# Kernel optimization log

Hardware: AMD Instinct MI355X
Metric: run time of the kernel (lower is better)

The kernel has to match this reference:

```python
import jax, jax.numpy as jnp
import numpy as np

NUM_EXPERT = 32
IN_FEAT = 256
OUT_FEAT = 256
TOTAL_TOKENS = 524288
CAPACITY = 16896  # static per-expert pad, > max expected count


def setup_inputs() -> dict:
    key = jax.random.key(0)
    k_inp, k_w = jax.random.split(key)
    inp = jax.random.normal(k_inp, (TOTAL_TOKENS, IN_FEAT), dtype=jnp.float32)
    # weight initialized like nn.Linear (kaiming-uniform-ish); scale of randn is fine for a numeric baseline
    weight = jax.random.normal(k_w, (NUM_EXPERT, OUT_FEAT, IN_FEAT), dtype=jnp.float32) * (1.0 / np.sqrt(IN_FEAT))
    # variable-sized expert groups summing exactly to TOTAL_TOKENS (tokens assumed pre-sorted by expert)
    rng = np.random.default_rng(0)
    counts = rng.multinomial(TOTAL_TOKENS, np.ones(NUM_EXPERT) / NUM_EXPERT)
    assert counts.max() <= CAPACITY and counts.sum() == TOTAL_TOKENS
    fwd_expert_count = jnp.asarray(counts, dtype=jnp.int64)
    return {"inp": inp, "weight": weight, "fwd_expert_count": fwd_expert_count, "capacity": CAPACITY}


def reference(inp, weight, fwd_expert_count, capacity):
    # Grouped GEMM: for expert e, out[seg_e] = inp[seg_e] @ weight[e].T
    E = weight.shape[0]
    T = inp.shape[0]
    counts = fwd_expert_count.astype(jnp.int32)
    cum = jnp.cumsum(counts)                       # [E] inclusive prefix sums
    starts = cum - counts                          # [E] segment starts
    tok = jnp.arange(T, dtype=jnp.int32)
    eid = jnp.searchsorted(cum, tok, side='right') # [T] expert id per token
    pos = tok - starts[eid]                        # [T] slot within expert group
    # Scatter tokens into padded per-expert buffer [E, capacity, in]
    buf = jnp.zeros((E, capacity, inp.shape[1]), dtype=inp.dtype).at[eid, pos].set(inp)
    # Batched matmul against per-expert weights [E, out, in] -> [E, capacity, out]
    y = jnp.einsum('eci,eoi->eco', buf, weight)
    # Gather back to token order [T, out]
    return y[eid, pos]
```

## Files before the change

kernel.cpp:

```cpp
#include <hip/hip_runtime.h>
#include <cstdint>
#include <cstddef>

#define NEXPERT 32
#define KIN 256
#define NOUT 256
#define NTOK 524288
#define BM 64

typedef float f32x4 __attribute__((ext_vector_type(4)));
typedef __bf16 bf16x8 __attribute__((ext_vector_type(8)));
typedef unsigned short u16;
typedef u16 u16x8 __attribute__((ext_vector_type(8)));

union BF8 { u16x8 u; bf16x8 b; };

__device__ __forceinline__ u16 f2bf(float f) {
  unsigned u = __float_as_uint(f);
  return (u16)((u + 0x7FFFu + ((u >> 16) & 1u)) >> 16);
}

__global__ void conv_w_kernel(const float* __restrict__ w, u16* __restrict__ wb) {
  const int i = (blockIdx.x * 256 + threadIdx.x) * 4;
  const float4 v = *reinterpret_cast<const float4*>(w + i);
  ushort4 o;
  o.x = f2bf(v.x); o.y = f2bf(v.y); o.z = f2bf(v.z); o.w = f2bf(v.w);
  *reinterpret_cast<ushort4*>(wb + i) = o;
}

__device__ __forceinline__ void gload(const float4* ap4, int ks, float4 (&v)[4]) {
#pragma unroll
  for (int i = 0; i < 4; ++i) v[i] = ap4[ks * 16 + i];
}

__device__ __forceinline__ void cvtw(const float4 (&v)[4], char* rbase, int cb, int rx) {
  u16x8 h0, h1;
  h0[0]=f2bf(v[0].x); h0[1]=f2bf(v[0].y); h0[2]=f2bf(v[0].z); h0[3]=f2bf(v[0].w);
  h0[4]=f2bf(v[1].x); h0[5]=f2bf(v[1].y); h0[6]=f2bf(v[1].z); h0[7]=f2bf(v[1].w);
  h1[0]=f2bf(v[2].x); h1[1]=f2bf(v[2].y); h1[2]=f2bf(v[2].z); h1[3]=f2bf(v[2].w);
  h1[4]=f2bf(v[3].x); h1[5]=f2bf(v[3].y); h1[6]=f2bf(v[3].z); h1[7]=f2bf(v[3].w);
  *reinterpret_cast<u16x8*>(rbase + ((cb     ) ^ rx)) = h0;
  *reinterpret_cast<u16x8*>(rbase + ((cb + 16) ^ rx)) = h1;
}

template<bool WSBF>
__device__ __forceinline__ void ldb(const u16* wB, const float* wF, int ks, BF8 (&dst)[4][2]) {
  if (WSBF) {
#pragma unroll
    for (int n = 0; n < 4; ++n)
#pragma unroll
      for (int kk = 0; kk < 2; ++kk)
        dst[n][kk].u = *reinterpret_cast<const u16x8*>(wB + n * (16 * KIN) + ks * 64 + kk * 32);
  } else {
#pragma unroll
    for (int n = 0; n < 4; ++n)
#pragma unroll
      for (int kk = 0; kk < 2; ++kk) {
        const float4* p = reinterpret_cast<const float4*>(wF + n * (16 * KIN) + ks * 64 + kk * 32);
        const float4 x = p[0], y = p[1];
        u16x8 h;
        h[0]=f2bf(x.x); h[1]=f2bf(x.y); h[2]=f2bf(x.z); h[3]=f2bf(x.w);
        h[4]=f2bf(y.x); h[5]=f2bf(y.y); h[6]=f2bf(y.z); h[7]=f2bf(y.w);
        dst[n][kk].u = h;
      }
  }
}

__device__ __forceinline__ void compute(const char* abase, int lg, int arx,
                                        const BF8 (&bfr)[4][2], f32x4 (&acc)[4][4]) {
#pragma unroll
  for (int kk = 0; kk < 2; ++kk) {
    BF8 af[4];
#pragma unroll
    for (int m = 0; m < 4; ++m)
      af[m].u = *reinterpret_cast<const u16x8*>(
          abase + m * 2048 + ((kk * 64 + (lg << 4)) ^ arx));
#pragma unroll
    for (int m = 0; m < 4; ++m)
#pragma unroll
      for (int n = 0; n < 4; ++n)
        acc[m][n] = __builtin_amdgcn_mfma_f32_16x16x32_bf16(
            af[m].b, bfr[n][kk].b, acc[m][n], 0, 0, 0);
  }
}

template<bool WSBF>
__global__ __launch_bounds__(256)
void moe_gemm_kernel(const float* __restrict__ inp,
                     const float* __restrict__ w32,
                     const u16* __restrict__ wbf,
                     const int* __restrict__ counts,
                     float* __restrict__ out)
{
  __shared__ u16 sA0[BM * 64];
  __shared__ u16 sA1[BM * 64];
  __shared__ int sCum[NEXPERT + 1];

  const int tid  = threadIdx.x;
  const int lane = tid & 63;
  const int wv   = tid >> 6;
  const int l15  = lane & 15;
  const int lg   = lane >> 4;

  if (tid < 32) {
    const long long* c64 = reinterpret_cast<const long long*>(counts);
    const long long p0 = c64[0];
    const bool is64 = (p0 >= 0 && p0 < (1ll << 31));
    int c = is64 ? (int)c64[tid] : counts[tid];
#pragma unroll
    for (int d = 1; d < 32; d <<= 1) {
      int o = __shfl_up(c, d, 64);
      if (tid >= d) c += o;
    }
    sCum[tid + 1] = c;
    if (tid == 0) sCum[0] = 0;
  }
  __syncthreads();

  const int t0 = blockIdx.x * BM;
  const int t1 = t0 + BM;

  int ee;
  {
    const int v = (lane < NEXPERT) ? sCum[lane + 1] : 0x7fffffff;
    const unsigned long long m = __ballot(v <= t0);
    ee = __popcll(m);
  }

  const int srow = tid >> 2;
  const int scol = (tid & 3) << 4;
  const float4* ap4 =
      reinterpret_cast<const float4*>(inp + (size_t)(t0 + srow) * KIN + scol);
  char* const r0 = reinterpret_cast<char*>(sA0) + srow * 128;
  char* const r1 = reinterpret_cast<char*>(sA1) + srow * 128;
  const int rx = (srow & 7) << 4;
  const int cb = scol << 1;
  const int arx = (l15 & 7) << 4;
  const char* const a0 = reinterpret_cast<const char*>(sA0) + l15 * 128;
  const char* const a1 = reinterpret_cast<const char*>(sA1) + l15 * 128;

  int rb = t0;
  int e = ee;
  while (rb < t1) {
    const int re = min(t1, sCum[e + 1]);
    if (re > rb) {
      const size_t wro = ((size_t)e << 16) + (size_t)((wv << 6) + l15) * KIN + lg * 8;
      const u16*   wB  = wbf + wro;
      const float* wF  = w32 + wro;

      f32x4 acc[4][4];
      const f32x4 zero = {0.f, 0.f, 0.f, 0.f};
#pragma unroll
      for (int m = 0; m < 4; ++m)
#pragma unroll
        for (int n = 0; n < 4; ++n) acc[m][n] = zero;

      float4 va[4], vb[4];
      BF8 bA[4][2], bB[4][2];

      gload(ap4, 0, va);
      gload(ap4, 1, vb);
      ldb<WSBF>(wB, wF, 0, bA);
      __syncthreads();
      cvtw(va, r0, cb, rx);
      __syncthreads();

      ldb<WSBF>(wB, wF, 1, bB); cvtw(vb, r1, cb, rx); gload(ap4, 2, va);
      compute(a0, lg, arx, bA, acc);
      __syncthreads();
      ldb<WSBF>(wB, wF, 2, bA); cvtw(va, r0, cb, rx); gload(ap4, 3, vb);
      compute(a1, lg, arx, bB, acc);
      __syncthreads();
      ldb<WSBF>(wB, wF, 3, bB); cvtw(vb, r1, cb, rx);
      compute(a0, lg, arx, bA, acc);
      __syncthreads();
      compute(a1, lg, arx, bB, acc);

      const bool full = (rb == t0) & (re == t1);
      if (full) {
#pragma unroll
        for (int m = 0; m < 4; ++m) {
          const int rbase = t0 + (m << 4) + (lg << 2);
#pragma unroll
          for (int n = 0; n < 4; ++n) {
            float* op = out + (size_t)rbase * NOUT + (wv << 6) + (n << 4) + l15;
#pragma unroll
            for (int j = 0; j < 4; ++j) op[(size_t)j * NOUT] = acc[m][n][j];
          }
        }
      } else {
#pragma unroll
        for (int m = 0; m < 4; ++m) {
          const int rbase = t0 + (m << 4) + (lg << 2);
#pragma unroll
          for (int n = 0; n < 4; ++n) {
            float* op = out + (size_t)rbase * NOUT + (wv << 6) + (n << 4) + l15;
#pragma unroll
            for (int j = 0; j < 4; ++j) {
              const int rg = rbase + j;
              if (rg >= rb && rg < re) op[(size_t)j * NOUT] = acc[m][n][j];
            }
          }
        }
      }
    }
    rb = re > rb ? re : rb;
    ++e;
  }
}

extern "C" void kernel_launch(void* const* d_in, const int* in_sizes, int n_in,
                              void* d_out, int out_size, void* d_ws, size_t ws_size,
                              hipStream_t stream) {
  const float* inp    = (const float*)d_in[0];
  const float* w      = (const float*)d_in[1];
  const int*   counts = (const int*)d_in[2];
  float*       out    = (float*)d_out;

  const size_t wbytes = (size_t)NEXPERT * NOUT * KIN * 2;
  const bool usews = (ws_size >= wbytes);

  if (usews) {
    u16* wbf = (u16*)d_ws;
    const int total = NEXPERT * NOUT * KIN;
    conv_w_kernel<<<total / (256 * 4), 256, 0, stream>>>(w, wbf);
    moe_gemm_kernel<true><<<NTOK / BM, 256, 0, stream>>>(inp, w, wbf, counts, out);
  } else {
    moe_gemm_kernel<false><<<NTOK / BM, 256, 0, stream>>>(inp, w, nullptr, counts, out);
  }
}
```

Measured before the change: 272.7 us.

## Load A fragments directly from global into registers, removing LDS staging and barriers

```diff
diff --git a/kernel.cpp b/kernel.cpp
--- a/kernel.cpp
+++ b/kernel.cpp
@@ -28,59 +28,32 @@
   *reinterpret_cast<ushort4*>(wb + i) = o;
 }
 
-__device__ __forceinline__ void gload(const float4* ap4, int ks, float4 (&v)[4]) {
-#pragma unroll
-  for (int i = 0; i < 4; ++i) v[i] = ap4[ks * 16 + i];
+__device__ __forceinline__ void cvt8(const float4& x, const float4& y, BF8& o) {
+  o.u[0]=f2bf(x.x); o.u[1]=f2bf(x.y); o.u[2]=f2bf(x.z); o.u[3]=f2bf(x.w);
+  o.u[4]=f2bf(y.x); o.u[5]=f2bf(y.y); o.u[6]=f2bf(y.z); o.u[7]=f2bf(y.w);
 }
 
-__device__ __forceinline__ void cvtw(const float4 (&v)[4], char* rbase, int cb, int rx) {
-  u16x8 h0, h1;
-  h0[0]=f2bf(v[0].x); h0[1]=f2bf(v[0].y); h0[2]=f2bf(v[0].z); h0[3]=f2bf(v[0].w);
-  h0[4]=f2bf(v[1].x); h0[5]=f2bf(v[1].y); h0[6]=f2bf(v[1].z); h0[7]=f2bf(v[1].w);
-  h1[0]=f2bf(v[2].x); h1[1]=f2bf(v[2].y); h1[2]=f2bf(v[2].z); h1[3]=f2bf(v[2].w);
-  h1[4]=f2bf(v[3].x); h1[5]=f2bf(v[3].y); h1[6]=f2bf(v[3].z); h1[7]=f2bf(v[3].w);
-  *reinterpret_cast<u16x8*>(rbase + ((cb     ) ^ rx)) = h0;
-  *reinterpret_cast<u16x8*>(rbase + ((cb + 16) ^ rx)) = h1;
+__device__ __forceinline__ void loadA(const float* aBase, int cch, float4 (&r)[8]) {
+#pragma unroll
+  for (int m = 0; m < 4; ++m) {
+    const float* p = aBase + (size_t)(m * 16) * KIN + cch * 32;
+    r[2*m]   = *reinterpret_cast<const float4*>(p);
+    r[2*m+1] = *reinterpret_cast<const float4*>(p + 4);
+  }
 }
 
 template<bool WSBF>
-__device__ __forceinline__ void ldb(const u16* wB, const float* wF, int ks, BF8 (&dst)[4][2]) {
+__device__ __forceinline__ void loadB(const u16* wB, const float* wF, int cch, BF8 (&d)[4]) {
   if (WSBF) {
 #pragma unroll
     for (int n = 0; n < 4; ++n)
-#pragma unroll
-      for (int kk = 0; kk < 2; ++kk)
-        dst[n][kk].u = *reinterpret_cast<const u16x8*>(wB + n * (16 * KIN) + ks * 64 + kk * 32);
+      d[n].u = *reinterpret_cast<const u16x8*>(wB + n * (16 * KIN) + cch * 32);
   } else {
 #pragma unroll
-    for (int n = 0; n < 4; ++n)
-#pragma unroll
-      for (int kk = 0; kk < 2; ++kk) {
-        const float4* p = reinterpret_cast<const float4*>(wF + n * (16 * KIN) + ks * 64 + kk * 32);
-        const float4 x = p[0], y = p[1];
-        u16x8 h;
-        h[0]=f2bf(x.x); h[1]=f2bf(x.y); h[2]=f2bf(x.z); h[3]=f2bf(x.w);
-        h[4]=f2bf(y.x); h[5]=f2bf(y.y); h[6]=f2bf(y.z); h[7]=f2bf(y.w);
-        dst[n][kk].u = h;
-      }
-  }
-}
-
-__device__ __forceinline__ void compute(const char* abase, int lg, int arx,
-                                        const BF8 (&bfr)[4][2], f32x4 (&acc)[4][4]) {
-#pragma unroll
-  for (int kk = 0; kk < 2; ++kk) {
-    BF8 af[4];
-#pragma unroll
-    for (int m = 0; m < 4; ++m)
-      af[m].u = *reinterpret_cast<const u16x8*>(
-          abase + m * 2048 + ((kk * 64 + (lg << 4)) ^ arx));
-#pragma unroll
-    for (int m = 0; m < 4; ++m)
-#pragma unroll
-      for (int n = 0; n < 4; ++n)
-        acc[m][n] = __builtin_amdgcn_mfma_f32_16x16x32_bf16(
-            af[m].b, bfr[n][kk].b, acc[m][n], 0, 0, 0);
+    for (int n = 0; n < 4; ++n) {
+      const float4* p = reinterpret_cast<const float4*>(wF + n * (16 * KIN) + cch * 32);
+      cvt8(p[0], p[1], d[n]);
+    }
   }
 }
 
@@ -92,57 +65,34 @@
                      const int* __restrict__ counts,
                      float* __restrict__ out)
 {
-  __shared__ u16 sA0[BM * 64];
-  __shared__ u16 sA1[BM * 64];
-  __shared__ int sCum[NEXPERT + 1];
-
   const int tid  = threadIdx.x;
   const int lane = tid & 63;
   const int wv   = tid >> 6;
   const int l15  = lane & 15;
   const int lg   = lane >> 4;
 
-  if (tid < 32) {
-    const long long* c64 = reinterpret_cast<const long long*>(counts);
-    const long long p0 = c64[0];
-    const bool is64 = (p0 >= 0 && p0 < (1ll << 31));
-    int c = is64 ? (int)c64[tid] : counts[tid];
+  const long long* c64 = reinterpret_cast<const long long*>(counts);
+  const long long p0 = c64[0];
+  const bool is64 = (p0 >= 0 && p0 < (1ll << 31));
+  int c = 0;
+  if (lane < 32) c = is64 ? (int)c64[lane] : counts[lane];
 #pragma unroll
-    for (int d = 1; d < 32; d <<= 1) {
-      int o = __shfl_up(c, d, 64);
-      if (tid >= d) c += o;
-    }
-    sCum[tid + 1] = c;
-    if (tid == 0) sCum[0] = 0;
+  for (int d = 1; d < 32; d <<= 1) {
+    const int o = __shfl_up(c, d, 64);
+    if (lane >= d) c += o;
   }
-  __syncthreads();
+  const int cum = (lane < 32) ? c : 0x7fffffff;
 
   const int t0 = blockIdx.x * BM;
   const int t1 = t0 + BM;
 
-  int ee;
-  {
-    const int v = (lane < NEXPERT) ? sCum[lane + 1] : 0x7fffffff;
-    const unsigned long long m = __ballot(v <= t0);
-    ee = __popcll(m);
-  }
-
-  const int srow = tid >> 2;
-  const int scol = (tid & 3) << 4;
-  const float4* ap4 =
-      reinterpret_cast<const float4*>(inp + (size_t)(t0 + srow) * KIN + scol);
-  char* const r0 = reinterpret_cast<char*>(sA0) + srow * 128;
-  char* const r1 = reinterpret_cast<char*>(sA1) + srow * 128;
-  const int rx = (srow & 7) << 4;
-  const int cb = scol << 1;
-  const int arx = (l15 & 7) << 4;
-  const char* const a0 = reinterpret_cast<const char*>(sA0) + l15 * 128;
-  const char* const a1 = reinterpret_cast<const char*>(sA1) + l15 * 128;
+  const float* aBase = inp + (size_t)(t0 + l15) * KIN + lg * 8;
 
   int rb = t0;
-  int e = ee;
+  int e  = __popcll(__ballot(cum <= t0));
+
   while (rb < t1) {
-    const int re = min(t1, sCum[e + 1]);
+    const int re = min(t1, __shfl(cum, e));
     if (re > rb) {
       const size_t wro = ((size_t)e << 16) + (size_t)((wv << 6) + l15) * KIN + lg * 8;
       const u16*   wB  = wbf + wro;
@@ -155,26 +105,31 @@
 #pragma unroll
         for (int n = 0; n < 4; ++n) acc[m][n] = zero;
 
-      float4 va[4], vb[4];
-      BF8 bA[4][2], bB[4][2];
+      float4 rawA[2][8];
+      BF8    bfr[2][4];
 
-      gload(ap4, 0, va);
-      gload(ap4, 1, vb);
-      ldb<WSBF>(wB, wF, 0, bA);
-      __syncthreads();
-      cvtw(va, r0, cb, rx);
-      __syncthreads();
+      loadA(aBase, 0, rawA[0]);
+      loadB<WSBF>(wB, wF, 0, bfr[0]);
 
-      ldb<WSBF>(wB, wF, 1, bB); cvtw(vb, r1, cb, rx); gload(ap4, 2, va);
-      compute(a0, lg, arx, bA, acc);
-      __syncthreads();
-      ldb<WSBF>(wB, wF, 2, bA); cvtw(va, r0, cb, rx); gload(ap4, 3, vb);
-      compute(a1, lg, arx, bB, acc);
-      __syncthreads();
-      ldb<WSBF>(wB, wF, 3, bB); cvtw(vb, r1, cb, rx);
-      compute(a0, lg, arx, bA, acc);
-      __syncthreads();
-      compute(a1, lg, arx, bB, acc);
+#pragma unroll
+      for (int cch = 0; cch < 8; ++cch) {
+        const int cur = cch & 1;
+        const int nxt = cur ^ 1;
+        if (cch < 7) {
+          loadA(aBase, cch + 1, rawA[nxt]);
+          loadB<WSBF>(wB, wF, cch + 1, bfr[nxt]);
+        }
+        BF8 af[4];
+#pragma unroll
+        for (int m = 0; m < 4; ++m)
+          cvt8(rawA[cur][2*m], rawA[cur][2*m+1], af[m]);
+#pragma unroll
+        for (int m = 0; m < 4; ++m)
+#pragma unroll
+          for (int n = 0; n < 4; ++n)
+            acc[m][n] = __builtin_amdgcn_mfma_f32_16x16x32_bf16(
+                af[m].b, bfr[cur][n].b, acc[m][n], 0, 0, 0);
+      }
 
       const bool full = (rb == t0) & (re == t1);
       if (full) {
```

After: 511.2 us. 87.5% more time.
